# Optimization experiments

Measured on AMD Instinct MI355X. Metric: run time of the kernel, lower is better.

Reference implementation:

```python
import jax, jax.numpy as jnp
import numpy as np

N = 100000
E = 1600000
D_IN = 128
D_H = 128
D_OUT = 40


def setup_inputs() -> dict:
    key = jax.random.key(0)
    ks = jax.random.split(key, 16)
    x = jax.random.normal(ks[0], (N, D_IN), dtype=jnp.float32)
    edge_src = jax.random.randint(ks[1], (E,), 0, N, dtype=jnp.int32)
    edge_dst = jax.random.randint(ks[2], (E,), 0, N, dtype=jnp.int32)

    def glorot(k, shape):
        fan_in, fan_out = shape[1], shape[0]
        lim = jnp.sqrt(6.0 / (fan_in + fan_out)).astype(jnp.float32)
        return jax.random.uniform(k, shape, jnp.float32, -lim, lim)

    # SAGEConv params: Wl acts on aggregated neighbors, Wr on root, plus bias.
    Wl0 = glorot(ks[3], (D_H, D_IN)); Wr0 = glorot(ks[4], (D_H, D_IN)); b0 = jnp.zeros((D_H,), jnp.float32)
    Wl1 = glorot(ks[5], (D_H, D_H));  Wr1 = glorot(ks[6], (D_H, D_H));  b1 = jnp.zeros((D_H,), jnp.float32)
    Wl2 = glorot(ks[7], (D_OUT, D_H)); Wr2 = glorot(ks[8], (D_OUT, D_H)); b2 = jnp.zeros((D_OUT,), jnp.float32)
    return {"x": x, "edge_src": edge_src, "edge_dst": edge_dst,
            "Wl0": Wl0, "Wr0": Wr0, "b0": b0,
            "Wl1": Wl1, "Wr1": Wr1, "b1": b1,
            "Wl2": Wl2, "Wr2": Wr2, "b2": b2}


def _mean_aggregate(x, edge_src, edge_dst, inv_deg):
    # adj_t @ x with mean reduce: sum neighbor feats into dst, divide by degree
    agg = jax.ops.segment_sum(x[edge_src], edge_dst, num_segments=N)
    return agg * inv_deg


def _sage_conv(x, edge_src, edge_dst, inv_deg, Wl, Wr, b):
    agg = _mean_aggregate(x, edge_src, edge_dst, inv_deg)
    return agg @ Wl.T + x @ Wr.T + b


def reference(x, edge_src, edge_dst, Wl0, Wr0, b0, Wl1, Wr1, b1, Wl2, Wr2, b2):
    deg = jax.ops.segment_sum(jnp.ones((E,), jnp.float32), edge_dst, num_segments=N)
    inv_deg = (1.0 / jnp.maximum(deg, 1.0))[:, None]  # [N,1]
    h = _sage_conv(x, edge_src, edge_dst, inv_deg, Wl0, Wr0, b0)
    h = jax.nn.relu(h)  # dropout is identity in eval mode
    h = _sage_conv(h, edge_src, edge_dst, inv_deg, Wl1, Wr1, b1)
    h = jax.nn.relu(h)
    h = _sage_conv(h, edge_src, edge_dst, inv_deg, Wl2, Wr2, b2)
    return jax.nn.log_softmax(h, axis=-1)
```

## Files before the change

### kernel.cpp

```cpp
#include <hip/hip_runtime.h>
#include <hip/hip_fp16.h>
#include <math.h>

#define NN 100000
#define NE 1600000
#define D 128
#define DOUT 40
#define NBUCK 391
#define CHUNK 4096
#define NCHUNK 391
#define LSTR 136

typedef _Float16 half8v __attribute__((ext_vector_type(8)));
typedef __attribute__((ext_vector_type(4))) float f32x4;

__device__ __forceinline__ unsigned packh(float a, float b) {
  return (unsigned)__half_as_ushort(__float2half_rn(a)) |
         ((unsigned)__half_as_ushort(__float2half_rn(b)) << 16);
}
__device__ __forceinline__ unsigned char f2fp8(float v) {
  return (unsigned char)(__builtin_amdgcn_cvt_pk_fp8_f32(v, v, 0, 0) & 0xff);
}
#define CVT2(u, s) __builtin_amdgcn_cvt_pk_f32_fp8((int)(u), s)
#define ACCR(v) { auto q = CVT2((v).x, 0); a[0] += q[0]; a[1] += q[1];   \
  q = CVT2((v).x, 1); a[2] += q[0];  a[3] += q[1];                        \
  q = CVT2((v).y, 0); a[4] += q[0];  a[5] += q[1];                        \
  q = CVT2((v).y, 1); a[6] += q[0];  a[7] += q[1];                        \
  q = CVT2((v).z, 0); a[8] += q[0];  a[9] += q[1];                        \
  q = CVT2((v).z, 1); a[10] += q[0]; a[11] += q[1];                       \
  q = CVT2((v).w, 0); a[12] += q[0]; a[13] += q[1];                       \
  q = CVT2((v).w, 1); a[14] += q[0]; a[15] += q[1]; }
#define ACCR8(v) { auto q = CVT2((v).x, 0); a[0] += q[0]; a[1] += q[1];  \
  q = CVT2((v).x, 1); a[2] += q[0]; a[3] += q[1];                         \
  q = CVT2((v).y, 0); a[4] += q[0]; a[5] += q[1];                         \
  q = CVT2((v).y, 1); a[6] += q[0]; a[7] += q[1]; }

__global__ void zero_kernel(int* __restrict__ p, int n) {
  int i = blockIdx.x * 256 + threadIdx.x;
  if (i < n) p[i] = 0;
}

__global__ __launch_bounds__(256) void cvt_kernel(const float* __restrict__ in,
                                                  _Float16* __restrict__ outh,
                                                  unsigned char* __restrict__ out8) {
  int i = (blockIdx.x * 256 + threadIdx.x) * 8;
  float4 v0 = *(const float4*)(in + i);
  float4 v1 = *(const float4*)(in + i + 4);
  uint4 oh;
  oh.x = packh(v0.x, v0.y);
  oh.y = packh(v0.z, v0.w);
  oh.z = packh(v1.x, v1.y);
  oh.w = packh(v1.z, v1.w);
  *(uint4*)(outh + i) = oh;
  unsigned w0 = __builtin_amdgcn_cvt_pk_fp8_f32(v0.x, v0.y, 0, 0);
  w0 = __builtin_amdgcn_cvt_pk_fp8_f32(v0.z, v0.w, w0, 1);
  unsigned w1 = __builtin_amdgcn_cvt_pk_fp8_f32(v1.x, v1.y, 0, 0);
  w1 = __builtin_amdgcn_cvt_pk_fp8_f32(v1.z, v1.w, w1, 1);
  *(uint2*)(out8 + i) = make_uint2(w0, w1);
}

__global__ __launch_bounds__(256) void bucket_hist_kernel(const int* __restrict__ dst,
                                                          int* __restrict__ bucket_cnt) {
  __shared__ int bc[NBUCK];
  int t = threadIdx.x;
  for (int i = t; i < NBUCK; i += 256) bc[i] = 0;
  __syncthreads();
  int e_base = blockIdx.x * CHUNK;
#pragma unroll
  for (int j = 0; j < 16; ++j) {
    int e = e_base + j * 256 + t;
    if (e < NE) atomicAdd(&bc[dst[e] >> 8], 1);
  }
  __syncthreads();
  for (int i = t; i < NBUCK; i += 256)
    if (bc[i]) atomicAdd(&bucket_cnt[i], bc[i]);
}

__global__ __launch_bounds__(512) void bucket_scan_kernel(const int* __restrict__ bucket_cnt,
                                                          int* __restrict__ bucket_base,
                                                          int* __restrict__ bucket_cursor) {
  __shared__ int s[512];
  int t = threadIdx.x;
  int c = (t < NBUCK) ? bucket_cnt[t] : 0;
  s[t] = c;
  __syncthreads();
  for (int off = 1; off < 512; off <<= 1) {
    int v = (t >= off) ? s[t - off] : 0;
    __syncthreads();
    s[t] += v;
    __syncthreads();
  }
  if (t < NBUCK) {
    int b = s[t] - c;
    bucket_base[t] = b;
    bucket_cursor[t] = b;
  }
  if (t == NBUCK) bucket_base[NBUCK] = s[NBUCK - 1];
}

__global__ __launch_bounds__(256) void binned_scatter_kernel(const int* __restrict__ src,
                                                             const int* __restrict__ dst,
                                                             int* __restrict__ bucket_cursor,
                                                             unsigned* __restrict__ pairs) {
  __shared__ int lcnt[NBUCK];
  __shared__ int lscan[NBUCK];
  __shared__ int gb[NBUCK];
  __shared__ unsigned ebuf[CHUNK];
  __shared__ unsigned short bbuf[CHUNK];
  int t = threadIdx.x;
  int e_base = blockIdx.x * CHUNK;
  for (int i = t; i < NBUCK; i += 256) lcnt[i] = 0;
  __syncthreads();

  int myb[16], myrank[16];
  unsigned mye[16];
#pragma unroll
  for (int j = 0; j < 16; ++j) {
    int e = e_base + j * 256 + t;
    if (e < NE) {
      int d = dst[e];
      mye[j] = (unsigned)src[e] | ((unsigned)(d & 255) << 24);
      myb[j] = d >> 8;
      myrank[j] = atomicAdd(&lcnt[d >> 8], 1);
    } else {
      myb[j] = -1;
    }
  }
  __syncthreads();

  lscan[t] = lcnt[t];
  if (256 + t < NBUCK) lscan[256 + t] = lcnt[256 + t];
  __syncthreads();
  for (int off = 1; off < 512; off <<= 1) {
    int v0 = (t >= off) ? lscan[t - off] : 0;
    int v1 = 0;
    int i1 = 256 + t;
    if (i1 < NBUCK) v1 = lscan[i1 - off];
    __syncthreads();
    if (t >= off) lscan[t] += v0;
    if (i1 < NBUCK) lscan[i1] += v1;
    __syncthreads();
  }

#pragma unroll
  for (int j = 0; j < 16; ++j)
    if (myb[j] >= 0) {
      int b = myb[j];
      int lpos = lscan[b] - lcnt[b] + myrank[j];
      ebuf[lpos] = mye[j];
      bbuf[lpos] = (unsigned short)b;
    }
  for (int i = t; i < NBUCK; i += 256)
    if (lcnt[i] > 0) gb[i] = atomicAdd(&bucket_cursor[i], lcnt[i]);
  __syncthreads();

  int chunk_n = min(CHUNK, NE - e_base);
  for (int s2 = t; s2 < chunk_n; s2 += 256) {
    int b = bbuf[s2];
    int g = gb[b] + (s2 - (lscan[b] - lcnt[b]));
    pairs[g] = ebuf[s2];
  }
}

__global__ __launch_bounds__(256) void bucket_build_kernel(const unsigned* __restrict__ pairs,
                                                           const int* __restrict__ bucket_base,
                                                           int* __restrict__ row_start,
                                                           int* __restrict__ nbr,
                                                           float* __restrict__ inv_deg) {
  __shared__ int cnt[256], loc[256], cur[256];
  int b = blockIdx.x;
  int t = threadIdx.x;
  int nbase = b << 8;
  int e0 = bucket_base[b], e1 = bucket_base[b + 1];
  cnt[t] = 0;
  __syncthreads();
  for (int e = e0 + t; e < e1; e += 256) {
    int d = (int)(pairs[e] >> 24);
    atomicAdd(&cnt[d], 1);
  }
  __syncthreads();
  loc[t] = cnt[t];
  __syncthreads();
  for (int off = 1; off < 256; off <<= 1) {
    int v = (t >= off) ? loc[t - off] : 0;
    __syncthreads();
    loc[t] += v;
    __syncthreads();
  }
  int excl = loc[t] - cnt[t];
  int node = nbase + t;
  if (node < NN) {
    row_start[node] = e0 + excl;
    inv_deg[node] = 1.0f / (float)(cnt[t] > 1 ? cnt[t] : 1);
  }
  cur[t] = excl;
  if (b == NBUCK - 1 && t == 0) row_start[NN] = NE;
  __syncthreads();
  for (int e = e0 + t; e < e1; e += 256) {
    unsigned pr = pairs[e];
    int d = (int)(pr >> 24);
    int p = atomicAdd(&cur[d], 1);
    nbr[e0 + p] = (int)(pr & 0xFFFFFFu);
  }
}

__global__ __launch_bounds__(256) void agg_kernel(const unsigned char* __restrict__ X8,
                                                  _Float16* __restrict__ out,
                                                  const int* __restrict__ row_start,
                                                  const int* __restrict__ nbr,
                                                  const float* __restrict__ inv_deg) {
  int g = blockIdx.x * 32 + (threadIdx.x >> 3);
  int ln = threadIdx.x & 7;
  if (g >= NN) return;
  int p0 = row_start[g];
  int p1 = row_start[g + 1];
  const uint4* base = (const uint4*)X8;
  float a[16];
#pragma unroll
  for (int i = 0; i < 16; ++i) a[i] = 0.f;
  int p = p0;
  for (; p + 3 < p1; p += 4) {
    int s0 = nbr[p], s1 = nbr[p + 1], s2 = nbr[p + 2], s3 = nbr[p + 3];
    uint4 v0 = base[(size_t)s0 * 8 + ln];
    uint4 v1 = base[(size_t)s1 * 8 + ln];
    uint4 v2 = base[(size_t)s2 * 8 + ln];
    uint4 v3 = base[(size_t)s3 * 8 + ln];
    ACCR(v0) ACCR(v1) ACCR(v2) ACCR(v3)
  }
  for (; p < p1; ++p) {
    uint4 v = base[(size_t)nbr[p] * 8 + ln];
    ACCR(v)
  }
  float id = inv_deg[g];
  uint4 o0, o1;
  o0.x = packh(a[0] * id, a[1] * id);
  o0.y = packh(a[2] * id, a[3] * id);
  o0.z = packh(a[4] * id, a[5] * id);
  o0.w = packh(a[6] * id, a[7] * id);
  o1.x = packh(a[8] * id, a[9] * id);
  o1.y = packh(a[10] * id, a[11] * id);
  o1.z = packh(a[12] * id, a[13] * id);
  o1.w = packh(a[14] * id, a[15] * id);
  uint4* ob = (uint4*)out;
  ob[(size_t)g * 16 + ln * 2] = o0;
  ob[(size_t)g * 16 + ln * 2 + 1] = o1;
}

__global__ __launch_bounds__(64) void prep_w_kernel(const float* __restrict__ Wl,
                                                    const float* __restrict__ Wr,
                                                    half8v* __restrict__ P) {
  int s = blockIdx.x >> 3;
  int n = blockIdx.x & 7;
  int l = threadIdx.x;
  int k0 = s * 32 + (l >> 4) * 8;
  int c = n * 16 + (l & 15);
  const float* W = (k0 < 128) ? Wl : Wr;
  int kb = (k0 < 128) ? k0 : k0 - 128;
  half8v h;
#pragma unroll
  for (int i = 0; i < 8; ++i) h[i] = (_Float16)W[c * 128 + kb + i];
  P[blockIdx.x * 64 + l] = h;
}

__global__ __launch_bounds__(64) void prep_wy2_kernel(const float* __restrict__ Wl,
                                                      const float* __restrict__ Wr,
                                                      half8v* __restrict__ P) {
  int s = blockIdx.x / 5;
  int n = blockIdx.x % 5;
  int l = threadIdx.x;
  int k0 = s * 32 + (l >> 4) * 8;
  int c = n * 16 + (l & 15);
  const float* W = (c < DOUT) ? Wl : Wr;
  int row = (c < DOUT) ? c : c - DOUT;
  half8v h;
#pragma unroll
  for (int i = 0; i < 8; ++i) h[i] = (_Float16)W[row * 128 + k0 + i];
  P[blockIdx.x * 64 + l] = h;
}

__global__ __launch_bounds__(256) void mfma_gemm_kernel(
    const _Float16* __restrict__ A, const _Float16* __restrict__ H,
    const half8v* __restrict__ B, const float* __restrict__ bias,
    _Float16* __restrict__ out, unsigned char* __restrict__ out8) {
  __shared__ _Float16 Os[128][LSTR];

  int t = threadIdx.x;
  int w = t >> 6, l = t & 63;
  int R0 = blockIdx.x * 128;
  int lc = l & 15;
  int lg = l >> 4;

  int frow = R0 + w * 32 + lc;
  int fr0 = min(frow, NN - 1);
  int fr1 = min(frow + 16, NN - 1);

  f32x4 acc[2][8];
#pragma unroll
  for (int m = 0; m < 2; ++m)
#pragma unroll
    for (int n = 0; n < 8; ++n) acc[m][n] = (f32x4){0.f, 0.f, 0.f, 0.f};

#pragma unroll
  for (int s = 0; s < 8; ++s) {
    const _Float16* src = (s < 4) ? A : H;
    int koff = (s & 3) * 32 + lg * 8;
    half8v ah0 = *(const half8v*)(src + (size_t)fr0 * D + koff);
    half8v ah1 = *(const half8v*)(src + (size_t)fr1 * D + koff);
    half8v bh[8];
#pragma unroll
    for (int n = 0; n < 8; ++n) bh[n] = B[(s * 8 + n) * 64 + l];
#pragma unroll
    for (int n = 0; n < 8; ++n) {
      acc[0][n] = __builtin_amdgcn_mfma_f32_16x16x32_f16(ah0, bh[n], acc[0][n], 0, 0, 0);
      acc[1][n] = __builtin_amdgcn_mfma_f32_16x16x32_f16(ah1, bh[n], acc[1][n], 0, 0, 0);
    }
  }

  float bcol[8];
#pragma unroll
  for (int n = 0; n < 8; ++n) bcol[n] = bias[n * 16 + lc];
#pragma unroll
  for (int m = 0; m < 2; ++m)
#pragma unroll
    for (int n = 0; n < 8; ++n) {
      int col = n * 16 + lc;
#pragma unroll
      for (int j = 0; j < 4; ++j) {
        int row = w * 32 + m * 16 + lg * 4 + j;
        Os[row][col] = (_Float16)fmaxf(acc[m][n][j] + bcol[n], 0.f);
      }
    }
  __syncthreads();

#pragma unroll
  for (int i = 0; i < 8; ++i) {
    int u = t + 256 * i;
    int row = u >> 4, seg = u & 15;
    int gr = R0 + row;
    if (gr < NN) {
      uint4 v = *(const uint4*)&Os[row][seg * 8];
      *(uint4*)(out + (size_t)gr * D + seg * 8) = v;
      if (out8) {
        unsigned w0 = __builtin_amdgcn_cvt_pk_fp8_f32(
            __half2float(__ushort_as_half((unsigned short)(v.x & 0xffff))),
            __half2float(__ushort_as_half((unsigned short)(v.x >> 16))), 0, 0);
        w0 = __builtin_amdgcn_cvt_pk_fp8_f32(
            __half2float(__ushort_as_half((unsigned short)(v.y & 0xffff))),
            __half2float(__ushort_as_half((unsigned short)(v.y >> 16))), w0, 1);
        unsigned w1 = __builtin_amdgcn_cvt_pk_fp8_f32(
            __half2float(__ushort_as_half((unsigned short)(v.z & 0xffff))),
            __half2float(__ushort_as_half((unsigned short)(v.z >> 16))), 0, 0);
        w1 = __builtin_amdgcn_cvt_pk_fp8_f32(
            __half2float(__ushort_as_half((unsigned short)(v.w & 0xffff))),
            __half2float(__ushort_as_half((unsigned short)(v.w >> 16))), w1, 1);
        *(uint2*)(out8 + (size_t)gr * D + seg * 8) = make_uint2(w0, w1);
      }
    }
  }
}

__global__ __launch_bounds__(256) void mfma_y2_kernel(
    const _Float16* __restrict__ H, const half8v* __restrict__ B,
    const float* __restrict__ b2,
    unsigned char* __restrict__ yl8, float* __restrict__ yr) {
  __shared__ unsigned char Y8[128][48];
  __shared__ float Yr[128][40];

  int t = threadIdx.x;
  int w = t >> 6, l = t & 63;
  int R0 = blockIdx.x * 128;
  int lc = l & 15;
  int lg = l >> 4;

  int frow = R0 + w * 32 + lc;
  int fr0 = min(frow, NN - 1);
  int fr1 = min(frow + 16, NN - 1);

  f32x4 acc[2][5];
#pragma unroll
  for (int m = 0; m < 2; ++m)
#pragma unroll
    for (int n = 0; n < 5; ++n) acc[m][n] = (f32x4){0.f, 0.f, 0.f, 0.f};

#pragma unroll
  for (int s = 0; s < 4; ++s) {
    int koff = s * 32 + lg * 8;
    half8v ah0 = *(const half8v*)(H + (size_t)fr0 * D + koff);
    half8v ah1 = *(const half8v*)(H + (size_t)fr1 * D + koff);
    half8v bh[5];
#pragma unroll
    for (int n = 0; n < 5; ++n) bh[n] = B[(s * 5 + n) * 64 + l];
#pragma unroll
    for (int n = 0; n < 5; ++n) {
      acc[0][n] = __builtin_amdgcn_mfma_f32_16x16x32_f16(ah0, bh[n], acc[0][n], 0, 0, 0);
      acc[1][n] = __builtin_amdgcn_mfma_f32_16x16x32_f16(ah1, bh[n], acc[1][n], 0, 0, 0);
    }
  }

#pragma unroll
  for (int m = 0; m < 2; ++m)
#pragma unroll
    for (int n = 0; n < 5; ++n) {
      int col = n * 16 + lc;
#pragma unroll
      for (int j = 0; j < 4; ++j) {
        int row = w * 32 + m * 16 + lg * 4 + j;
        float v = acc[m][n][j];
        if (col < DOUT) {
          Y8[row][col] = f2fp8(v);
        } else {
          Yr[row][col - DOUT] = v + b2[col - DOUT];
        }
      }
    }
  if (t < 128) *(uint2*)&Y8[t][40] = make_uint2(0, 0);
  __syncthreads();

#pragma unroll
  for (int i = 0; i < 3; ++i) {
    int u = t + 256 * i;
    int row = u / 6, seg = u % 6;
    int gr = R0 + row;
    if (gr < NN) *(uint2*)(yl8 + (size_t)gr * 48 + seg * 8) = *(const uint2*)&Y8[row][seg * 8];
  }
#pragma unroll
  for (int i = 0; i < 5; ++i) {
    int u = t + 256 * i;
    int row = u / 10, seg = u % 10;
    int gr = R0 + row;
    if (gr < NN) *(float4*)(yr + (size_t)gr * DOUT + seg * 4) = *(const float4*)&Yr[row][seg * 4];
  }
}

__global__ __launch_bounds__(256) void agg_out_kernel(const unsigned char* __restrict__ yl8,
                                                      const float* __restrict__ yr,
                                                      const int* __restrict__ row_start,
                                                      const int* __restrict__ nbr,
                                                      const float* __restrict__ inv_deg,
                                                      float* __restrict__ out) {
  int g = blockIdx.x * 32 + (threadIdx.x >> 3);
  int ln = threadIdx.x & 7;
  if (g >= NN) return;
  int lnc = (ln < 6) ? ln : 5;
  int p0 = row_start[g];
  int p1 = row_start[g + 1];
  const uint2* base = (const uint2*)yl8;
  float a[8];
#pragma unroll
  for (int i = 0; i < 8; ++i) a[i] = 0.f;
  int p = p0;
  for (; p + 3 < p1; p += 4) {
    int s0 = nbr[p], s1 = nbr[p + 1], s2 = nbr[p + 2], s3 = nbr[p + 3];
    uint2 v0 = base[(size_t)s0 * 6 + lnc];
    uint2 v1 = base[(size_t)s1 * 6 + lnc];
    uint2 v2 = base[(size_t)s2 * 6 + lnc];
    uint2 v3 = base[(size_t)s3 * 6 + lnc];
    ACCR8(v0) ACCR8(v1) ACCR8(v2) ACCR8(v3)
  }
  for (; p < p1; ++p) {
    uint2 v = base[(size_t)nbr[p] * 6 + lnc];
    ACCR8(v)
  }
  float id = inv_deg[g];
  float z[8];
#pragma unroll
  for (int i = 0; i < 8; ++i) z[i] = a[i] * id;
  bool valid = (ln < 5);
  if (valid) {
    float4 r0 = *(const float4*)(yr + (size_t)g * DOUT + ln * 8);
    float4 r1 = *(const float4*)(yr + (size_t)g * DOUT + ln * 8 + 4);
    z[0] += r0.x; z[1] += r0.y; z[2] += r0.z; z[3] += r0.w;
    z[4] += r1.x; z[5] += r1.y; z[6] += r1.z; z[7] += r1.w;
  }
  float zm = -INFINITY;
  if (valid)
#pragma unroll
    for (int i = 0; i < 8; ++i) zm = fmaxf(zm, z[i]);
#pragma unroll
  for (int off = 1; off < 8; off <<= 1) zm = fmaxf(zm, __shfl_xor(zm, off, 8));
  float ssum = 0.f;
  if (valid)
#pragma unroll
    for (int i = 0; i < 8; ++i) ssum += expf(z[i] - zm);
#pragma unroll
  for (int off = 1; off < 8; off <<= 1) ssum += __shfl_xor(ssum, off, 8);
  float lse = zm + logf(ssum);
  if (valid) {
    float4 o0 = make_float4(z[0] - lse, z[1] - lse, z[2] - lse, z[3] - lse);
    float4 o1 = make_float4(z[4] - lse, z[5] - lse, z[6] - lse, z[7] - lse);
    *(float4*)(out + (size_t)g * DOUT + ln * 8) = o0;
    *(float4*)(out + (size_t)g * DOUT + ln * 8 + 4) = o1;
  }
}

extern "C" void kernel_launch(void* const* d_in, const int* in_sizes, int n_in,
                              void* d_out, int out_size, void* d_ws, size_t ws_size,
                              hipStream_t stream) {
  const float* x   = (const float*)d_in[0];
  const int* esrc  = (const int*)d_in[1];
  const int* edst  = (const int*)d_in[2];
  const float* Wl0 = (const float*)d_in[3];
  const float* Wr0 = (const float*)d_in[4];
  const float* b0  = (const float*)d_in[5];
  const float* Wl1 = (const float*)d_in[6];
  const float* Wr1 = (const float*)d_in[7];
  const float* b1  = (const float*)d_in[8];
  const float* Wl2 = (const float*)d_in[9];
  const float* Wr2 = (const float*)d_in[10];
  const float* b2  = (const float*)d_in[11];
  float* out = (float*)d_out;

  char* ws = (char*)d_ws;
  size_t off = 0;
  auto carve = [&](size_t bytes) -> char* {
    char* p = ws + off;
    off = (off + bytes + 255) & ~(size_t)255;
    return p;
  };
  int* bucket_cnt    = (int*)carve((size_t)NBUCK * 4);
  int* bucket_base   = (int*)carve((size_t)(NBUCK + 1) * 4);
  int* bucket_cursor = (int*)carve((size_t)NBUCK * 4);
  int* row_start     = (int*)carve((size_t)(NN + 1) * 4);
  int* nbr           = (int*)carve((size_t)NE * 4);
  float* inv_deg     = (float*)carve((size_t)NN * 4);
  unsigned* pairs    = (unsigned*)carve((size_t)NE * 4);
  half8v* B0         = (half8v*)carve((size_t)64 * 64 * 16);
  half8v* B1         = (half8v*)carve((size_t)64 * 64 * 16);
  half8v* By2        = (half8v*)carve((size_t)20 * 64 * 16);
  _Float16* xb   = (_Float16*)carve((size_t)NN * D * 2);
  unsigned char* x8    = (unsigned char*)carve((size_t)NN * D);
  _Float16* bufA = (_Float16*)carve((size_t)NN * D * 2);
  _Float16* bufB = (_Float16*)carve((size_t)NN * D * 2);
  unsigned char* bufB8 = (unsigned char*)carve((size_t)NN * D);
  _Float16* bufC = (_Float16*)carve((size_t)NN * D * 2);
  unsigned char* yl8   = (unsigned char*)carve((size_t)NN * 48);
  float* yr      = (float*)carve((size_t)NN * DOUT * 4);
  if (off > ws_size) return;

  const int GRID_AGG = (NN + 31) / 32;
  const int GRID_GEMM = (NN + 127) / 128;
  const int GRID_CVT = NN * D / 8 / 256;
  const int GRID_AO = (NN + 31) / 32;

  zero_kernel<<<2, 256, 0, stream>>>(bucket_cnt, NBUCK);
  bucket_hist_kernel<<<NCHUNK, 256, 0, stream>>>(edst, bucket_cnt);
  bucket_scan_kernel<<<1, 512, 0, stream>>>(bucket_cnt, bucket_base, bucket_cursor);
  binned_scatter_kernel<<<NCHUNK, 256, 0, stream>>>(esrc, edst, bucket_cursor, pairs);
  bucket_build_kernel<<<NBUCK, 256, 0, stream>>>(pairs, bucket_base, row_start, nbr, inv_deg);

  cvt_kernel<<<GRID_CVT, 256, 0, stream>>>(x, xb, x8);
  prep_w_kernel<<<64, 64, 0, stream>>>(Wl0, Wr0, B0);
  prep_w_kernel<<<64, 64, 0, stream>>>(Wl1, Wr1, B1);
  prep_wy2_kernel<<<20, 64, 0, stream>>>(Wl2, Wr2, By2);

  agg_kernel<<<GRID_AGG, 256, 0, stream>>>(x8, bufA, row_start, nbr, inv_deg);
  mfma_gemm_kernel<<<GRID_GEMM, 256, 0, stream>>>(bufA, xb, B0, b0, bufB, bufB8);
  agg_kernel<<<GRID_AGG, 256, 0, stream>>>(bufB8, bufA, row_start, nbr, inv_deg);
  mfma_gemm_kernel<<<GRID_GEMM, 256, 0, stream>>>(bufA, bufB, B1, b1, bufC, nullptr);
  mfma_y2_kernel<<<GRID_GEMM, 256, 0, stream>>>(bufC, By2, b2, yl8, yr);
  agg_out_kernel<<<GRID_AO, 256, 0, stream>>>(yl8, yr, row_start, nbr, inv_deg, out);
}
```

Baseline: 231.7 us.

## Fuse neighbor aggregation into SAGE GEMM via shared memory; pad fp8 output rows to 64 bytes

Result: slower. 264.8 us (+14.3%).

```diff
diff --git a/kernel.cpp b/kernel.cpp
--- a/kernel.cpp
+++ b/kernel.cpp
@@ -204,48 +204,6 @@
   }
 }
 
-__global__ __launch_bounds__(256) void agg_kernel(const unsigned char* __restrict__ X8,
-                                                  _Float16* __restrict__ out,
-                                                  const int* __restrict__ row_start,
-                                                  const int* __restrict__ nbr,
-                                                  const float* __restrict__ inv_deg) {
-  int g = blockIdx.x * 32 + (threadIdx.x >> 3);
-  int ln = threadIdx.x & 7;
-  if (g >= NN) return;
-  int p0 = row_start[g];
-  int p1 = row_start[g + 1];
-  const uint4* base = (const uint4*)X8;
-  float a[16];
-#pragma unroll
-  for (int i = 0; i < 16; ++i) a[i] = 0.f;
-  int p = p0;
-  for (; p + 3 < p1; p += 4) {
-    int s0 = nbr[p], s1 = nbr[p + 1], s2 = nbr[p + 2], s3 = nbr[p + 3];
-    uint4 v0 = base[(size_t)s0 * 8 + ln];
-    uint4 v1 = base[(size_t)s1 * 8 + ln];
-    uint4 v2 = base[(size_t)s2 * 8 + ln];
-    uint4 v3 = base[(size_t)s3 * 8 + ln];
-    ACCR(v0) ACCR(v1) ACCR(v2) ACCR(v3)
-  }
-  for (; p < p1; ++p) {
-    uint4 v = base[(size_t)nbr[p] * 8 + ln];
-    ACCR(v)
-  }
-  float id = inv_deg[g];
-  uint4 o0, o1;
-  o0.x = packh(a[0] * id, a[1] * id);
-  o0.y = packh(a[2] * id, a[3] * id);
-  o0.z = packh(a[4] * id, a[5] * id);
-  o0.w = packh(a[6] * id, a[7] * id);
-  o1.x = packh(a[8] * id, a[9] * id);
-  o1.y = packh(a[10] * id, a[11] * id);
-  o1.z = packh(a[12] * id, a[13] * id);
-  o1.w = packh(a[14] * id, a[15] * id);
-  uint4* ob = (uint4*)out;
-  ob[(size_t)g * 16 + ln * 2] = o0;
-  ob[(size_t)g * 16 + ln * 2 + 1] = o1;
-}
-
 __global__ __launch_bounds__(64) void prep_w_kernel(const float* __restrict__ Wl,
                                                     const float* __restrict__ Wr,
                                                     half8v* __restrict__ P) {
@@ -278,11 +236,13 @@
   P[blockIdx.x * 64 + l] = h;
 }
 
-__global__ __launch_bounds__(256) void mfma_gemm_kernel(
-    const _Float16* __restrict__ A, const _Float16* __restrict__ H,
+__global__ __launch_bounds__(256) void fused_gemm_kernel(
+    const unsigned char* __restrict__ X8, const _Float16* __restrict__ H,
+    const int* __restrict__ row_start, const int* __restrict__ nbr,
+    const float* __restrict__ inv_deg,
     const half8v* __restrict__ B, const float* __restrict__ bias,
     _Float16* __restrict__ out, unsigned char* __restrict__ out8) {
-  __shared__ _Float16 Os[128][LSTR];
+  __shared__ _Float16 As[128][LSTR];
 
   int t = threadIdx.x;
   int w = t >> 6, l = t & 63;
@@ -290,6 +250,50 @@
   int lc = l & 15;
   int lg = l >> 4;
 
+  {
+    int ln = t & 7;
+    const uint4* base = (const uint4*)X8;
+#pragma unroll
+    for (int it = 0; it < 4; ++it) {
+      int lrow = it * 32 + (t >> 3);
+      int g = R0 + lrow;
+      float a[16];
+#pragma unroll
+      for (int i = 0; i < 16; ++i) a[i] = 0.f;
+      float id = 0.f;
+      if (g < NN) {
+        int p0 = row_start[g];
+        int p1 = row_start[g + 1];
+        int p = p0;
+        for (; p + 3 < p1; p += 4) {
+          int s0 = nbr[p], s1 = nbr[p + 1], s2 = nbr[p + 2], s3 = nbr[p + 3];
+          uint4 v0 = base[(size_t)s0 * 8 + ln];
+          uint4 v1 = base[(size_t)s1 * 8 + ln];
+          uint4 v2 = base[(size_t)s2 * 8 + ln];
+          uint4 v3 = base[(size_t)s3 * 8 + ln];
+          ACCR(v0) ACCR(v1) ACCR(v2) ACCR(v3)
+        }
+        for (; p < p1; ++p) {
+          uint4 v = base[(size_t)nbr[p] * 8 + ln];
+          ACCR(v)
+        }
+        id = inv_deg[g];
+      }
+      uint4 o0, o1;
+      o0.x = packh(a[0] * id, a[1] * id);
+      o0.y = packh(a[2] * id, a[3] * id);
+      o0.z = packh(a[4] * id, a[5] * id);
+      o0.w = packh(a[6] * id, a[7] * id);
+      o1.x = packh(a[8] * id, a[9] * id);
+      o1.y = packh(a[10] * id, a[11] * id);
+      o1.z = packh(a[12] * id, a[13] * id);
+      o1.w = packh(a[14] * id, a[15] * id);
+      *(uint4*)&As[lrow][ln * 16] = o0;
+      *(uint4*)&As[lrow][ln * 16 + 8] = o1;
+    }
+  }
+  __syncthreads();
+
   int frow = R0 + w * 32 + lc;
   int fr0 = min(frow, NN - 1);
   int fr1 = min(frow + 16, NN - 1);
@@ -302,10 +306,15 @@
 
 #pragma unroll
   for (int s = 0; s < 8; ++s) {
-    const _Float16* src = (s < 4) ? A : H;
     int koff = (s & 3) * 32 + lg * 8;
-    half8v ah0 = *(const half8v*)(src + (size_t)fr0 * D + koff);
-    half8v ah1 = *(const half8v*)(src + (size_t)fr1 * D + koff);
+    half8v ah0, ah1;
+    if (s < 4) {
+      ah0 = *(const half8v*)&As[w * 32 + lc][koff];
+      ah1 = *(const half8v*)&As[w * 32 + 16 + lc][koff];
+    } else {
+      ah0 = *(const half8v*)(H + (size_t)fr0 * D + koff);
+      ah1 = *(const half8v*)(H + (size_t)fr1 * D + koff);
+    }
     half8v bh[8];
 #pragma unroll
     for (int n = 0; n < 8; ++n) bh[n] = B[(s * 8 + n) * 64 + l];
@@ -315,6 +324,7 @@
       acc[1][n] = __builtin_amdgcn_mfma_f32_16x16x32_f16(ah1, bh[n], acc[1][n], 0, 0, 0);
     }
   }
+  __syncthreads();
 
   float bcol[8];
 #pragma unroll
@@ -327,7 +337,7 @@
 #pragma unroll
       for (int j = 0; j < 4; ++j) {
         int row = w * 32 + m * 16 + lg * 4 + j;
-        Os[row][col] = (_Float16)fmaxf(acc[m][n][j] + bcol[n], 0.f);
+        As[row][col] = (_Float16)fmaxf(acc[m][n][j] + bcol[n], 0.f);
       }
     }
   __syncthreads();
@@ -338,7 +348,7 @@
     int row = u >> 4, seg = u & 15;
     int gr = R0 + row;
     if (gr < NN) {
-      uint4 v = *(const uint4*)&Os[row][seg * 8];
+      uint4 v = *(const uint4*)&As[row][seg * 8];
       *(uint4*)(out + (size_t)gr * D + seg * 8) = v;
       if (out8) {
         unsigned w0 = __builtin_amdgcn_cvt_pk_fp8_f32(
@@ -363,7 +373,7 @@
     const _Float16* __restrict__ H, const half8v* __restrict__ B,
     const float* __restrict__ b2,
     unsigned char* __restrict__ yl8, float* __restrict__ yr) {
-  __shared__ unsigned char Y8[128][48];
+  __shared__ unsigned char Y8[128][64];
   __shared__ float Yr[128][40];
 
   int t = threadIdx.x;
@@ -413,15 +423,19 @@
         }
       }
     }
-  if (t < 128) *(uint2*)&Y8[t][40] = make_uint2(0, 0);
-  __syncthreads();
-
-#pragma unroll
-  for (int i = 0; i < 3; ++i) {
+  if (t < 128) {
+    *(uint2*)&Y8[t][40] = make_uint2(0, 0);
+    *(uint2*)&Y8[t][48] = make_uint2(0, 0);
+    *(uint2*)&Y8[t][56] = make_uint2(0, 0);
+  }
+  __syncthreads();
+
+#pragma unroll
+  for (int i = 0; i < 4; ++i) {
     int u = t + 256 * i;
-    int row = u / 6, seg = u % 6;
+    int row = u >> 3, seg = u & 7;
     int gr = R0 + row;
-    if (gr < NN) *(uint2*)(yl8 + (size_t)gr * 48 + seg * 8) = *(const uint2*)&Y8[row][seg * 8];
+    if (gr < NN) *(uint2*)(yl8 + (size_t)gr * 64 + seg * 8) = *(const uint2*)&Y8[row][seg * 8];
   }
 #pragma unroll
   for (int i = 0; i < 5; ++i) {
@@ -441,7 +455,6 @@
   int g = blockIdx.x * 32 + (threadIdx.x >> 3);
   int ln = threadIdx.x & 7;
   if (g >= NN) return;
-  int lnc = (ln < 6) ? ln : 5;
   int p0 = row_start[g];
   int p1 = row_start[g + 1];
   const uint2* base = (const uint2*)yl8;
@@ -451,14 +464,14 @@
   int p = p0;
   for (; p + 3 < p1; p += 4) {
     int s0 = nbr[p], s1 = nbr[p + 1], s2 = nbr[p + 2], s3 = nbr[p + 3];
-    uint2 v0 = base[(size_t)s0 * 6 + lnc];
-    uint2 v1 = base[(size_t)s1 * 6 + lnc];
-    uint2 v2 = base[(size_t)s2 * 6 + lnc];
-    uint2 v3 = base[(size_t)s3 * 6 + lnc];
+    uint2 v0 = base[(size_t)s0 * 8 + ln];
+    uint2 v1 = base[(size_t)s1 * 8 + ln];
+    uint2 v2 = base[(size_t)s2 * 8 + ln];
+    uint2 v3 = base[(size_t)s3 * 8 + ln];
     ACCR8(v0) ACCR8(v1) ACCR8(v2) ACCR8(v3)
   }
   for (; p < p1; ++p) {
-    uint2 v = base[(size_t)nbr[p] * 6 + lnc];
+    uint2 v = base[(size_t)nbr[p] * 8 + ln];
     ACCR8(v)
   }
   float id = inv_deg[g];
@@ -529,15 +542,13 @@
   half8v* By2        = (half8v*)carve((size_t)20 * 64 * 16);
   _Float16* xb   = (_Float16*)carve((size_t)NN * D * 2);
   unsigned char* x8    = (unsigned char*)carve((size_t)NN * D);
-  _Float16* bufA = (_Float16*)carve((size_t)NN * D * 2);
   _Float16* bufB = (_Float16*)carve((size_t)NN * D * 2);
   unsigned char* bufB8 = (unsigned char*)carve((size_t)NN * D);
   _Float16* bufC = (_Float16*)carve((size_t)NN * D * 2);
-  unsigned char* yl8   = (unsigned char*)carve((size_t)NN * 48);
+  unsigned char* yl8   = (unsigned char*)carve((size_t)NN * 64);
   float* yr      = (float*)carve((size_t)NN * DOUT * 4);
   if (off > ws_size) return;
 
-  const int GRID_AGG = (NN + 31) / 32;
   const int GRID_GEMM = (NN + 127) / 128;
   const int GRID_CVT = NN * D / 8 / 256;
   const int GRID_AO = (NN + 31) / 32;
@@ -553,10 +564,10 @@
   prep_w_kernel<<<64, 64, 0, stream>>>(Wl1, Wr1, B1);
   prep_wy2_kernel<<<20, 64, 0, stream>>>(Wl2, Wr2, By2);
 
-  agg_kernel<<<GRID_AGG, 256, 0, stream>>>(x8, bufA, row_start, nbr, inv_deg);
-  mfma_gemm_kernel<<<GRID_GEMM, 256, 0, stream>>>(bufA, xb, B0, b0, bufB, bufB8);
-  agg_kernel<<<GRID_AGG, 256, 0, stream>>>(bufB8, bufA, row_start, nbr, inv_deg);
-  mfma_gemm_kernel<<<GRID_GEMM, 256, 0, stream>>>(bufA, bufB, B1, b1, bufC, nullptr);
+  fused_gemm_kernel<<<GRID_GEMM, 256, 0, stream>>>(x8, xb, row_start, nbr, inv_deg,
+                                                   B0, b0, bufB, bufB8);
+  fused_gemm_kernel<<<GRID_GEMM, 256, 0, stream>>>(bufB8, bufB, row_start, nbr, inv_deg,
+                                                   B1, b1, bufC, nullptr);
   mfma_y2_kernel<<<GRID_GEMM, 256, 0, stream>>>(bufC, By2, b2, yl8, yr);
   agg_out_kernel<<<GRID_AO, 256, 0, stream>>>(yl8, yr, row_start, nbr, inv_deg, out);
 }
```
